# Kernel tuning notes

Hardware: AMD Instinct MI355X
Metric: run time of the kernel (lower is better)

## Reference

```python
import jax, jax.numpy as jnp
import numpy as np

B, S, D = 2, 2048, 1024
H, DH = 16, 64
EPS = 1e-5

def setup_inputs() -> dict:
    key = jax.random.key(0)
    ks = jax.random.split(key, 8)
    s = 0.02
    return {
        "x": jax.random.normal(ks[0], (B, S, D), dtype=jnp.float32),
        "ln_gamma": jnp.ones((D,), jnp.float32),
        "ln_beta": jnp.zeros((D,), jnp.float32),
        "wq": jax.random.normal(ks[1], (D, H * DH), jnp.float32) * s,
        "bq": jnp.zeros((H * DH,), jnp.float32),
        "wk": jax.random.normal(ks[2], (D, H * DH), jnp.float32) * s,
        "bk": jnp.zeros((H * DH,), jnp.float32),
        "wv": jax.random.normal(ks[3], (D, H * DH), jnp.float32) * s,
        "bv": jnp.zeros((H * DH,), jnp.float32),
        "wo": jax.random.normal(ks[4], (H * DH, D), jnp.float32) * s,
        "bo": jnp.zeros((D,), jnp.float32),
    }

def reference(x, ln_gamma, ln_beta, wq, bq, wk, bk, wv, bv, wo, bo):
    # Pre-LayerNorm over d_model
    mu = jnp.mean(x, axis=-1, keepdims=True)
    var = jnp.var(x, axis=-1, keepdims=True)
    xn = (x - mu) * jax.lax.rsqrt(var + EPS) * ln_gamma + ln_beta

    b, s, _ = xn.shape
    q = (xn @ wq + bq).reshape(b, s, H, DH)
    k = (xn @ wk + bk).reshape(b, s, H, DH)
    v = (xn @ wv + bv).reshape(b, s, H, DH)

    scale = jnp.sqrt(jnp.float32(DH))
    scores = jnp.einsum('bihd,bjhd->bhij', q, k) / scale  # [b,h,s,s]
    att = jax.nn.softmax(scores, axis=-1)
    out = jnp.einsum('bhij,bjhd->bihd', att, v).reshape(b, s, H * DH)
    return out @ wo + bo
```

## Files before the change

kernel.cpp:

```cpp
#include <hip/hip_runtime.h>
#include <math.h>

#define SEQ   2048
#define DM    1024
#define NHEAD 16
#define HD    64
#define NTOK  4096
#define EPS   1e-5f
#define SCALE_C 0.18033688f

typedef __attribute__((ext_vector_type(8))) short v8s;
typedef __attribute__((ext_vector_type(4))) short v4s;
typedef __attribute__((ext_vector_type(4))) float v4f;
typedef unsigned short ushort_t;

#define GLOAD16(g, l) __builtin_amdgcn_global_load_lds( \
    (const __attribute__((address_space(1))) unsigned int*)(g), \
    (__attribute__((address_space(3))) unsigned int*)(l), 16, 0, 0)

#if defined(__has_builtin)
#if __has_builtin(__builtin_amdgcn_mfma_f32_16x16x16_bf16)
#define MFMA16(va, vb, vc) __builtin_amdgcn_mfma_f32_16x16x16_bf16(va, vb, vc, 0, 0, 0)
#elif __has_builtin(__builtin_amdgcn_mfma_f32_16x16x16bf16_1k)
#define MFMA16(va, vb, vc) __builtin_amdgcn_mfma_f32_16x16x16bf16_1k(va, vb, vc, 0, 0, 0)
#endif
#endif
#ifndef MFMA16
__device__ __forceinline__ v4f mfma16_asm(v4s a, v4s b, v4f c) {
  asm volatile("s_nop 2\n\tv_mfma_f32_16x16x16_bf16 %0, %1, %2, %0\n\ts_nop 4"
               : "+v"(c) : "v"(a), "v"(b));
  return c;
}
#define MFMA16(va, vb, vc) mfma16_asm(va, vb, vc)
#endif

__device__ __forceinline__ unsigned short f2bf(float f) {
  union { float f; unsigned u; } v; v.f = f;
  unsigned r = v.u + 0x7FFFu + ((v.u >> 16) & 1u);
  return (unsigned short)(r >> 16);
}

__device__ __forceinline__ unsigned pack2_bf16(float a, float b) {
  union { float f; unsigned u; } ua, ub;
  ua.f = a; ub.f = b;
  return __builtin_amdgcn_perm(ub.u + 0x8000u, ua.u + 0x8000u, 0x07060302u);
}

__global__ __launch_bounds__(256) void prep_kernel(
    const float* __restrict__ x, const float* __restrict__ g,
    const float* __restrict__ be, ushort_t* __restrict__ y,
    const float* __restrict__ w0, const float* __restrict__ w1,
    const float* __restrict__ w2, const float* __restrict__ w3,
    ushort_t* __restrict__ o0, ushort_t* __restrict__ o1,
    ushort_t* __restrict__ o2, ushort_t* __restrict__ o3) {
  __shared__ float red[8];
  __shared__ float mu_s, rs_s;
  __shared__ float tile[64][65];
  const int t = threadIdx.x;
  if (blockIdx.x < NTOK) {
    const int row = blockIdx.x;
    const float4 v = ((const float4*)(x + (size_t)row * DM))[t];
    float s  = v.x + v.y + v.z + v.w;
    float ss = v.x*v.x + v.y*v.y + v.z*v.z + v.w*v.w;
    #pragma unroll
    for (int off = 32; off > 0; off >>= 1) {
      s  += __shfl_down(s,  off, 64);
      ss += __shfl_down(ss, off, 64);
    }
    const int wid = t >> 6, lane = t & 63;
    if (lane == 0) { red[wid] = s; red[4 + wid] = ss; }
    __syncthreads();
    if (t == 0) {
      const float S  = red[0] + red[1] + red[2] + red[3];
      const float SS = red[4] + red[5] + red[6] + red[7];
      const float mu  = S * (1.0f / DM);
      const float var = SS * (1.0f / DM) - mu * mu;
      mu_s = mu; rs_s = rsqrtf(var + EPS);
    }
    __syncthreads();
    const float mu = mu_s, r = rs_s;
    const float4 gv = ((const float4*)g)[t];
    const float4 bv = ((const float4*)be)[t];
    ushort4 o;
    o.x = f2bf((v.x - mu) * r * gv.x + bv.x);
    o.y = f2bf((v.y - mu) * r * gv.y + bv.y);
    o.z = f2bf((v.z - mu) * r * gv.z + bv.z);
    o.w = f2bf((v.w - mu) * r * gv.w + bv.w);
    *(ushort4*)(y + (size_t)row * DM + t * 4) = o;
  } else {
    const int i = blockIdx.x - NTOK;
    const int z = i >> 8;
    const float* w = (z==0) ? w0 : (z==1) ? w1 : (z==2) ? w2 : w3;
    ushort_t* o    = (z==0) ? o0 : (z==1) ? o1 : (z==2) ? o2 : o3;
    const int n0 = (i & 15) * 64, k0 = ((i >> 4) & 15) * 64;
    const int r = t >> 4, c4 = (t & 15) * 4;
    #pragma unroll
    for (int ii = 0; ii < 4; ++ii) {
      const float4 v = *(const float4*)(w + (size_t)(k0 + r + ii*16) * DM + n0 + c4);
      tile[r + ii*16][c4 + 0] = v.x;
      tile[r + ii*16][c4 + 1] = v.y;
      tile[r + ii*16][c4 + 2] = v.z;
      tile[r + ii*16][c4 + 3] = v.w;
    }
    __syncthreads();
    #pragma unroll
    for (int ii = 0; ii < 4; ++ii) {
      const int n = r + ii*16;
      ushort4 o4;
      o4.x = f2bf(tile[c4 + 0][n]);
      o4.y = f2bf(tile[c4 + 1][n]);
      o4.z = f2bf(tile[c4 + 2][n]);
      o4.w = f2bf(tile[c4 + 3][n]);
      *(ushort4*)(o + (size_t)(n0 + n) * DM + k0 + c4) = o4;
    }
  }
}

__device__ __forceinline__ void gemm_main(ushort_t* lsa, ushort_t* lsb,
    const ushort_t* A, const ushort_t* WT, int m0, int n0, v4f acc[4][4]) {
  const int tid = threadIdx.x;
  const int wid = tid >> 6, lane = tid & 63;
  const int mh = (wid & 1) << 6, nh = (wid >> 1) << 6;
  const int r16 = lane & 15, quad = lane >> 4;
  const int srow = lane >> 2, sch = lane & 3;
  for (int k0 = 0; k0 < DM; k0 += 64) {
    __syncthreads();
    #pragma unroll
    for (int s = 0; s < 2; ++s) {
      #pragma unroll
      for (int j = 0; j < 2; ++j) {
        const int o = wid * 2 + j;
        GLOAD16(A  + (size_t)(m0 + o*16 + srow) * DM + k0 + s*32 + sch*8, lsa + s*4096 + o*512);
        GLOAD16(WT + (size_t)(n0 + o*16 + srow) * DM + k0 + s*32 + sch*8, lsb + s*4096 + o*512);
      }
    }
    __syncthreads();
    #pragma unroll
    for (int s = 0; s < 2; ++s) {
      v8s af[4], bfr[4];
      #pragma unroll
      for (int i = 0; i < 4; ++i) {
        af[i]  = *(const v8s*)(lsa + s*4096 + (mh + i*16 + r16)*32 + quad*8);
        bfr[i] = *(const v8s*)(lsb + s*4096 + (nh + i*16 + r16)*32 + quad*8);
      }
      #pragma unroll
      for (int i = 0; i < 4; ++i)
        #pragma unroll
        for (int j = 0; j < 4; ++j)
          acc[i][j] = __builtin_amdgcn_mfma_f32_16x16x32_bf16(af[i], bfr[j], acc[i][j], 0, 0, 0);
    }
  }
}

__global__ __launch_bounds__(256, 2) void gemm_qkv(const ushort_t* __restrict__ xn,
    const ushort_t* __restrict__ wtq, const ushort_t* __restrict__ wtk, const ushort_t* __restrict__ wtv,
    const float* __restrict__ bq, const float* __restrict__ bk, const float* __restrict__ bv,
    ushort_t* __restrict__ qo, ushort_t* __restrict__ ko, ushort_t* __restrict__ vto) {
  __shared__ ushort_t lsa[128*64];
  __shared__ ushort_t lsb[128*64];
  const int flat = blockIdx.x;
  const int nf = (flat & 7) * 96 + (flat >> 3);
  const int zi = nf >> 8;
  const int yi = (nf >> 3) & 31;
  const int xi = nf & 7;
  const ushort_t* WT = (zi == 0) ? wtq : (zi == 1) ? wtk : wtv;
  const float* bias  = (zi == 0) ? bq  : (zi == 1) ? bk  : bv;
  const int m0 = yi * 128, n0 = xi * 128;
  v4f acc[4][4];
  #pragma unroll
  for (int i = 0; i < 4; ++i)
    #pragma unroll
    for (int j = 0; j < 4; ++j) acc[i][j] = (v4f){0.f, 0.f, 0.f, 0.f};
  gemm_main(lsa, lsb, xn, WT, m0, n0, acc);
  const int tid = threadIdx.x, wid = tid >> 6, lane = tid & 63;
  const int mh = (wid & 1) << 6, nh = (wid >> 1) << 6;
  const int r16 = lane & 15, quad = lane >> 4;
  if (zi < 2) {
    ushort_t* out = (zi == 0) ? qo : ko;
    const float sc = (zi == 0) ? SCALE_C : 1.0f;
    #pragma unroll
    for (int bn = 0; bn < 4; ++bn) {
      const int col = n0 + nh + bn*16 + r16;
      const float bb = bias[col];
      #pragma unroll
      for (int am = 0; am < 4; ++am) {
        const int tb = m0 + mh + am*16 + quad*4;
        #pragma unroll
        for (int r = 0; r < 4; ++r)
          out[(size_t)(tb + r) * DM + col] = f2bf((acc[am][bn][r] + bb) * sc);
      }
    }
  } else {
    #pragma unroll
    for (int bn = 0; bn < 4; ++bn) {
      const int col = n0 + nh + bn*16 + r16;
      const float bb = bias[col];
      const int h = col >> 6, d = col & 63;
      #pragma unroll
      for (int am = 0; am < 4; ++am) {
        const int tb = m0 + mh + am*16 + quad*4;
        const int b = tb >> 11, t = tb & 2047;
        const int bh = b * NHEAD + h;
        ushort4 o4;
        o4.x = f2bf(acc[am][bn][0] + bb);
        o4.y = f2bf(acc[am][bn][1] + bb);
        o4.z = f2bf(acc[am][bn][2] + bb);
        o4.w = f2bf(acc[am][bn][3] + bb);
        const size_t idx = (size_t)bh * 131072 + (size_t)(t >> 6) * 4096 +
                           (size_t)((((t >> 4) & 3) * 4) + (d >> 4)) * 256 +
                           ((t >> 2) & 3) * 64 + (d & 15) * 4;
        *(ushort4*)(vto + idx) = o4;
      }
    }
  }
}

__global__ __launch_bounds__(256, 2) void gemm_out(const ushort_t* __restrict__ A,
    const ushort_t* __restrict__ WT, const float* __restrict__ bias,
    float* __restrict__ out) {
  __shared__ ushort_t lsa[128*64];
  __shared__ ushort_t lsb[64*64];
  const int flat = blockIdx.x;
  const int nf = (flat & 7) * 64 + (flat >> 3);
  const int n0 = (nf & 15) * 64, m0 = (nf >> 4) * 128;
  const int tid = threadIdx.x;
  const int wid = tid >> 6, lane = tid & 63;
  const int mh = (wid & 1) << 6, nh = (wid >> 1) << 5;
  const int r16 = lane & 15, quad = lane >> 4;
  const int srow = lane >> 2, sch = lane & 3;
  v4f acc[4][2];
  #pragma unroll
  for (int i = 0; i < 4; ++i)
    #pragma unroll
    for (int j = 0; j < 2; ++j) acc[i][j] = (v4f){0.f, 0.f, 0.f, 0.f};
  for (int k0 = 0; k0 < DM; k0 += 64) {
    __syncthreads();
    #pragma unroll
    for (int s = 0; s < 2; ++s) {
      #pragma unroll
      for (int j = 0; j < 2; ++j) {
        const int o = wid * 2 + j;
        GLOAD16(A + (size_t)(m0 + o*16 + srow) * DM + k0 + s*32 + sch*8, lsa + s*4096 + o*512);
      }
      GLOAD16(WT + (size_t)(n0 + wid*16 + srow) * DM + k0 + s*32 + sch*8, lsb + s*2048 + wid*512);
    }
    __syncthreads();
    #pragma unroll
    for (int s = 0; s < 2; ++s) {
      v8s af[4], bfr[2];
      #pragma unroll
      for (int i = 0; i < 4; ++i)
        af[i] = *(const v8s*)(lsa + s*4096 + (mh + i*16 + r16)*32 + quad*8);
      #pragma unroll
      for (int j = 0; j < 2; ++j)
        bfr[j] = *(const v8s*)(lsb + s*2048 + (nh + j*16 + r16)*32 + quad*8);
      #pragma unroll
      for (int i = 0; i < 4; ++i)
        #pragma unroll
        for (int j = 0; j < 2; ++j)
          acc[i][j] = __builtin_amdgcn_mfma_f32_16x16x32_bf16(af[i], bfr[j], acc[i][j], 0, 0, 0);
    }
  }
  #pragma unroll
  for (int bn = 0; bn < 2; ++bn) {
    const int col = n0 + nh + bn*16 + r16;
    const float bb = bias[col];
    #pragma unroll
    for (int am = 0; am < 4; ++am) {
      const int tb = m0 + mh + am*16 + quad*4;
      #pragma unroll
      for (int r = 0; r < 4; ++r)
        out[(size_t)(tb + r) * DM + col] = acc[am][bn][r] + bb;
    }
  }
}

#define OHALF ((size_t)32 * 2048 * 64)
#define LHALF (32 * 2048)
template<int SPLIT>
__global__ __launch_bounds__(256, 8) void attn_kernel(
    const ushort_t* __restrict__ Q, const ushort_t* __restrict__ K,
    const ushort_t* __restrict__ Vt, ushort_t* __restrict__ O,
    float* __restrict__ Opart, float* __restrict__ lpart) {
  __shared__ ushort_t kbuf[8*512];
  __shared__ ushort_t vbuf[8*512];
  const int tid = threadIdx.x, wid = tid >> 6, lane = tid & 63;
  const int r16 = lane & 15, quad = lane >> 4;
  const int q0 = blockIdx.x * 64, bh = blockIdx.y;
  const int half = SPLIT ? blockIdx.z : 0;
  const int b = bh >> 4, h = bh & 15;
  const ushort_t* gQ = Q + (size_t)b * SEQ * DM + h * HD;
  const ushort_t* gK = K + (size_t)b * SEQ * DM + h * HD;
  const ushort_t* gV = Vt + (size_t)bh * 131072;

  const int qtok = q0 + wid * 16 + r16;
  const v8s qf0 = *(const v8s*)(gQ + (size_t)qtok * DM + quad * 8);
  const v8s qf1 = *(const v8s*)(gQ + (size_t)qtok * DM + 32 + quad * 8);
  v4f acco[4];
  #pragma unroll
  for (int i = 0; i < 4; ++i) acco[i] = (v4f){0.f, 0.f, 0.f, 0.f};
  float lrun = 0.f;

  const int NIT = SPLIT ? (SEQ / 128) : (SEQ / 64);
  const int kt0 = half * NIT;
  const int o0 = wid * 2, o1 = wid * 2 + 1;
  const ushort_t* srcK0 = gK + (size_t)((o0 >> 1) * 16 + r16) * DM + (o0 & 1) * 32 + quad * 8;
  const ushort_t* srcK1 = gK + (size_t)((o1 >> 1) * 16 + r16) * DM + (o1 & 1) * 32 + quad * 8;
  const ushort_t* srcV  = gV + lane * 8;

  {
    const int k0 = kt0 * 64;
    GLOAD16(srcK0 + (size_t)k0 * DM, kbuf + o0 * 512);
    GLOAD16(srcK1 + (size_t)k0 * DM, kbuf + o1 * 512);
    GLOAD16(srcV + (size_t)kt0 * 4096 + o0 * 512, vbuf + o0 * 512);
    GLOAD16(srcV + (size_t)kt0 * 4096 + o1 * 512, vbuf + o1 * 512);
  }
  __syncthreads();

  for (int it = 0; it < NIT; ++it) {
    const int kt = kt0 + it;
    uint4 rk0, rk1, rv0, rv1;
    const bool pf = (it + 1 < NIT);
    if (pf) {
      const size_t k0n = (size_t)(kt + 1) * 64;
      rk0 = *(const uint4*)(srcK0 + k0n * DM);
      rk1 = *(const uint4*)(srcK1 + k0n * DM);
      rv0 = *(const uint4*)(srcV + (size_t)(kt + 1) * 4096 + o0 * 512);
      rv1 = *(const uint4*)(srcV + (size_t)(kt + 1) * 4096 + o1 * 512);
    }

    v4f sacc[4];
    #pragma unroll
    for (int g = 0; g < 4; ++g) sacc[g] = (v4f){0.f, 0.f, 0.f, 0.f};
    #pragma unroll
    for (int g = 0; g < 4; ++g) {
      const v8s ka0 = *(const v8s*)(kbuf + (g*2 + 0) * 512 + lane * 8);
      const v8s ka1 = *(const v8s*)(kbuf + (g*2 + 1) * 512 + lane * 8);
      sacc[g] = __builtin_amdgcn_mfma_f32_16x16x32_bf16(ka0, qf0, sacc[g], 0, 0, 0);
      sacc[g] = __builtin_amdgcn_mfma_f32_16x16x32_bf16(ka1, qf1, sacc[g], 0, 0, 0);
    }

    float ls = 0.f;
    v4s pfrag[4];
    #pragma unroll
    for (int g = 0; g < 4; ++g) {
      float e0 = __builtin_amdgcn_exp2f(sacc[g][0]);
      float e1 = __builtin_amdgcn_exp2f(sacc[g][1]);
      float e2 = __builtin_amdgcn_exp2f(sacc[g][2]);
      float e3 = __builtin_amdgcn_exp2f(sacc[g][3]);
      ls += (e0 + e1) + (e2 + e3);
      union { v4s s; uint2 u; } pk;
      pk.u.x = pack2_bf16(e0, e1);
      pk.u.y = pack2_bf16(e2, e3);
      pfrag[g] = pk.s;
    }
    ls += __shfl_xor(ls, 16, 64);
    ls += __shfl_xor(ls, 32, 64);
    lrun += ls;

    #pragma unroll
    for (int dg = 0; dg < 4; ++dg) {
      #pragma unroll
      for (int g = 0; g < 4; ++g) {
        const v4s vf = *(const v4s*)(vbuf + (g*4 + dg) * 256 + quad * 64 + r16 * 4);
        acco[dg] = MFMA16(vf, pfrag[g], acco[dg]);
      }
    }

    __syncthreads();
    if (pf) {
      *(uint4*)(kbuf + o0 * 512 + lane * 8) = rk0;
      *(uint4*)(kbuf + o1 * 512 + lane * 8) = rk1;
      *(uint4*)(vbuf + o0 * 512 + lane * 8) = rv0;
      *(uint4*)(vbuf + o1 * 512 + lane * 8) = rv1;
    }
    __syncthreads();
  }

  if (SPLIT) {
    float* Op = Opart + half * OHALF + ((size_t)bh * SEQ + qtok) * 64;
    #pragma unroll
    for (int dg = 0; dg < 4; ++dg)
      *(v4f*)(Op + dg*16 + quad*4) = acco[dg];
    if (quad == 0) lpart[half * LHALF + bh * SEQ + qtok] = lrun;
  } else {
    const float inv = 1.f / lrun;
    ushort_t* gO = O + (size_t)b * SEQ * DM + h * HD;
    #pragma unroll
    for (int dg = 0; dg < 4; ++dg) {
      ushort4 o4;
      o4.x = f2bf(acco[dg][0] * inv);
      o4.y = f2bf(acco[dg][1] * inv);
      o4.z = f2bf(acco[dg][2] * inv);
      o4.w = f2bf(acco[dg][3] * inv);
      *(ushort4*)(gO + (size_t)qtok * DM + dg*16 + quad*4) = o4;
    }
  }
}

__global__ __launch_bounds__(256) void combine_kernel(
    const float* __restrict__ Opart, const float* __restrict__ lpart,
    ushort_t* __restrict__ ob) {
  const int tok = blockIdx.x;
  const int b = tok >> 11, t = tok & 2047;
  const int dm0 = threadIdx.x * 4;
  const int h = dm0 >> 6, d = dm0 & 63;
  const int bh = b * NHEAD + h;
  const size_t idx = ((size_t)bh * SEQ + t) * 64 + d;
  const float4 a = *(const float4*)(Opart + idx);
  const float4 c = *(const float4*)(Opart + OHALF + idx);
  const float l = lpart[bh * SEQ + t] + lpart[LHALF + bh * SEQ + t];
  const float inv = 1.f / l;
  ushort4 o4;
  o4.x = f2bf((a.x + c.x) * inv);
  o4.y = f2bf((a.y + c.y) * inv);
  o4.z = f2bf((a.z + c.z) * inv);
  o4.w = f2bf((a.w + c.w) * inv);
  *(ushort4*)(ob + (size_t)tok * DM + dm0) = o4;
}

extern "C" void kernel_launch(void* const* d_in, const int* in_sizes, int n_in,
                              void* d_out, int out_size, void* d_ws, size_t ws_size,
                              hipStream_t stream) {
  const float* x     = (const float*)d_in[0];
  const float* gamma = (const float*)d_in[1];
  const float* beta  = (const float*)d_in[2];
  const float* wq    = (const float*)d_in[3];
  const float* bq    = (const float*)d_in[4];
  const float* wk    = (const float*)d_in[5];
  const float* bk    = (const float*)d_in[6];
  const float* wv    = (const float*)d_in[7];
  const float* bv    = (const float*)d_in[8];
  const float* wo    = (const float*)d_in[9];
  const float* bo    = (const float*)d_in[10];
  float* out = (float*)d_out;

  unsigned char* w8 = (unsigned char*)d_ws;
  const size_t MB = 1024 * 1024;
  ushort_t* xn  = (ushort_t*)(w8 + 0 * MB);
  ushort_t* qb  = (ushort_t*)(w8 + 8 * MB);
  ushort_t* kb  = (ushort_t*)(w8 + 16 * MB);
  ushort_t* vt  = (ushort_t*)(w8 + 24 * MB);
  ushort_t* wtq = (ushort_t*)(w8 + 32 * MB);
  ushort_t* wtk = (ushort_t*)(w8 + 34 * MB);
  ushort_t* wtv = (ushort_t*)(w8 + 36 * MB);
  ushort_t* wto = (ushort_t*)(w8 + 38 * MB);
  float* Opart  = (float*)(w8 + 40 * MB);
  float* lpart  = (float*)(w8 + 72 * MB);
  ushort_t* ob  = xn;

  prep_kernel<<<dim3(NTOK + 1024), dim3(256), 0, stream>>>(
      x, gamma, beta, xn, wq, wk, wv, wo, wtq, wtk, wtv, wto);
  gemm_qkv<<<dim3(768), dim3(256), 0, stream>>>(xn, wtq, wtk, wtv, bq, bk, bv, qb, kb, vt);
  if (ws_size >= 73 * MB) {
    attn_kernel<1><<<dim3(SEQ / 64, 2 * NHEAD, 2), dim3(256), 0, stream>>>(
        qb, kb, vt, nullptr, Opart, lpart);
    combine_kernel<<<dim3(NTOK), dim3(256), 0, stream>>>(Opart, lpart, ob);
  } else {
    attn_kernel<0><<<dim3(SEQ / 64, 2 * NHEAD, 1), dim3(256), 0, stream>>>(
        qb, kb, vt, ob, nullptr, nullptr);
  }
  gemm_out<<<dim3(512), dim3(256), 0, stream>>>(ob, wto, bo, out);
}
```

Before: 207.2 us.

## Process two query tiles per wave to reuse K/V LDS loads, drop register prefetch

Each wave now handles 32 query rows (two 16-row fragments) instead of 16, so each K/V tile loaded into LDS feeds twice as many MFMAs, and the grid is halved in x. The register-staged prefetch of the next K/V tile is replaced by a direct global_load_lds at the top of each iteration, bracketed by two barriers. The occupancy hint is lowered from 8 to 4 blocks per CU to allow the larger register footprint. This halves the K/V global and LDS traffic per query, at the cost of exposing load latency each iteration, since nothing overlaps it any more, and of fewer resident waves and blocks.

```diff
diff --git a/kernel.cpp b/kernel.cpp
--- a/kernel.cpp
+++ b/kernel.cpp
@@ -278,7 +278,7 @@
 #define OHALF ((size_t)32 * 2048 * 64)
 #define LHALF (32 * 2048)
 template<int SPLIT>
-__global__ __launch_bounds__(256, 8) void attn_kernel(
+__global__ __launch_bounds__(256, 4) void attn_kernel(
     const ushort_t* __restrict__ Q, const ushort_t* __restrict__ K,
     const ushort_t* __restrict__ Vt, ushort_t* __restrict__ O,
     float* __restrict__ Opart, float* __restrict__ lpart) {
@@ -286,20 +286,26 @@
   __shared__ ushort_t vbuf[8*512];
   const int tid = threadIdx.x, wid = tid >> 6, lane = tid & 63;
   const int r16 = lane & 15, quad = lane >> 4;
-  const int q0 = blockIdx.x * 64, bh = blockIdx.y;
+  const int q0 = blockIdx.x * 128, bh = blockIdx.y;
   const int half = SPLIT ? blockIdx.z : 0;
   const int b = bh >> 4, h = bh & 15;
   const ushort_t* gQ = Q + (size_t)b * SEQ * DM + h * HD;
   const ushort_t* gK = K + (size_t)b * SEQ * DM + h * HD;
   const ushort_t* gV = Vt + (size_t)bh * 131072;
 
-  const int qtok = q0 + wid * 16 + r16;
-  const v8s qf0 = *(const v8s*)(gQ + (size_t)qtok * DM + quad * 8);
-  const v8s qf1 = *(const v8s*)(gQ + (size_t)qtok * DM + 32 + quad * 8);
-  v4f acco[4];
+  const int qt0 = q0 + wid * 32 + r16;
+  const int qt1 = qt0 + 16;
+  const v8s qf00 = *(const v8s*)(gQ + (size_t)qt0 * DM + quad * 8);
+  const v8s qf01 = *(const v8s*)(gQ + (size_t)qt0 * DM + 32 + quad * 8);
+  const v8s qf10 = *(const v8s*)(gQ + (size_t)qt1 * DM + quad * 8);
+  const v8s qf11 = *(const v8s*)(gQ + (size_t)qt1 * DM + 32 + quad * 8);
+  v4f acc0[4], acc1[4];
   #pragma unroll
-  for (int i = 0; i < 4; ++i) acco[i] = (v4f){0.f, 0.f, 0.f, 0.f};
-  float lrun = 0.f;
+  for (int i = 0; i < 4; ++i) {
+    acc0[i] = (v4f){0.f, 0.f, 0.f, 0.f};
+    acc1[i] = (v4f){0.f, 0.f, 0.f, 0.f};
+  }
+  float lrun0 = 0.f, lrun1 = 0.f;
 
   const int NIT = SPLIT ? (SEQ / 128) : (SEQ / 64);
   const int kt0 = half * NIT;
@@ -308,92 +314,102 @@
   const ushort_t* srcK1 = gK + (size_t)((o1 >> 1) * 16 + r16) * DM + (o1 & 1) * 32 + quad * 8;
   const ushort_t* srcV  = gV + lane * 8;
 
-  {
-    const int k0 = kt0 * 64;
+  for (int it = 0; it < NIT; ++it) {
+    const int kt = kt0 + it;
+    const int k0 = kt * 64;
+    __syncthreads();
     GLOAD16(srcK0 + (size_t)k0 * DM, kbuf + o0 * 512);
     GLOAD16(srcK1 + (size_t)k0 * DM, kbuf + o1 * 512);
-    GLOAD16(srcV + (size_t)kt0 * 4096 + o0 * 512, vbuf + o0 * 512);
-    GLOAD16(srcV + (size_t)kt0 * 4096 + o1 * 512, vbuf + o1 * 512);
-  }
-  __syncthreads();
-
-  for (int it = 0; it < NIT; ++it) {
-    const int kt = kt0 + it;
-    uint4 rk0, rk1, rv0, rv1;
-    const bool pf = (it + 1 < NIT);
-    if (pf) {
-      const size_t k0n = (size_t)(kt + 1) * 64;
-      rk0 = *(const uint4*)(srcK0 + k0n * DM);
-      rk1 = *(const uint4*)(srcK1 + k0n * DM);
-      rv0 = *(const uint4*)(srcV + (size_t)(kt + 1) * 4096 + o0 * 512);
-      rv1 = *(const uint4*)(srcV + (size_t)(kt + 1) * 4096 + o1 * 512);
-    }
-
-    v4f sacc[4];
-    #pragma unroll
-    for (int g = 0; g < 4; ++g) sacc[g] = (v4f){0.f, 0.f, 0.f, 0.f};
+    GLOAD16(srcV + (size_t)kt * 4096 + o0 * 512, vbuf + o0 * 512);
+    GLOAD16(srcV + (size_t)kt * 4096 + o1 * 512, vbuf + o1 * 512);
+    __syncthreads();
+
+    v4f s0[4], s1[4];
+    #pragma unroll
+    for (int g = 0; g < 4; ++g) {
+      s0[g] = (v4f){0.f, 0.f, 0.f, 0.f};
+      s1[g] = (v4f){0.f, 0.f, 0.f, 0.f};
+    }
     #pragma unroll
     for (int g = 0; g < 4; ++g) {
       const v8s ka0 = *(const v8s*)(kbuf + (g*2 + 0) * 512 + lane * 8);
       const v8s ka1 = *(const v8s*)(kbuf + (g*2 + 1) * 512 + lane * 8);
-      sacc[g] = __builtin_amdgcn_mfma_f32_16x16x32_bf16(ka0, qf0, sacc[g], 0, 0, 0);
-      sacc[g] = __builtin_amdgcn_mfma_f32_16x16x32_bf16(ka1, qf1, sacc[g], 0, 0, 0);
-    }
-
-    float ls = 0.f;
-    v4s pfrag[4];
+      s0[g] = __builtin_amdgcn_mfma_f32_16x16x32_bf16(ka0, qf00, s0[g], 0, 0, 0);
+      s0[g] = __builtin_amdgcn_mfma_f32_16x16x32_bf16(ka1, qf01, s0[g], 0, 0, 0);
+      s1[g] = __builtin_amdgcn_mfma_f32_16x16x32_bf16(ka0, qf10, s1[g], 0, 0, 0);
+      s1[g] = __builtin_amdgcn_mfma_f32_16x16x32_bf16(ka1, qf11, s1[g], 0, 0, 0);
+    }
+
+    v4s pf0[4], pf1[4];
+    float ls0 = 0.f, ls1 = 0.f;
     #pragma unroll
     for (int g = 0; g < 4; ++g) {
-      float e0 = __builtin_amdgcn_exp2f(sacc[g][0]);
-      float e1 = __builtin_amdgcn_exp2f(sacc[g][1]);
-      float e2 = __builtin_amdgcn_exp2f(sacc[g][2]);
-      float e3 = __builtin_amdgcn_exp2f(sacc[g][3]);
-      ls += (e0 + e1) + (e2 + e3);
+      float e0 = __builtin_amdgcn_exp2f(s0[g][0]);
+      float e1 = __builtin_amdgcn_exp2f(s0[g][1]);
+      float e2 = __builtin_amdgcn_exp2f(s0[g][2]);
+      float e3 = __builtin_amdgcn_exp2f(s0[g][3]);
+      ls0 += (e0 + e1) + (e2 + e3);
       union { v4s s; uint2 u; } pk;
       pk.u.x = pack2_bf16(e0, e1);
       pk.u.y = pack2_bf16(e2, e3);
-      pfrag[g] = pk.s;
-    }
-    ls += __shfl_xor(ls, 16, 64);
-    ls += __shfl_xor(ls, 32, 64);
-    lrun += ls;
+      pf0[g] = pk.s;
+      float f0 = __builtin_amdgcn_exp2f(s1[g][0]);
+      float f1 = __builtin_amdgcn_exp2f(s1[g][1]);
+      float f2 = __builtin_amdgcn_exp2f(s1[g][2]);
+      float f3 = __builtin_amdgcn_exp2f(s1[g][3]);
+      ls1 += (f0 + f1) + (f2 + f3);
+      union { v4s s; uint2 u; } pk2;
+      pk2.u.x = pack2_bf16(f0, f1);
+      pk2.u.y = pack2_bf16(f2, f3);
+      pf1[g] = pk2.s;
+    }
+    ls0 += __shfl_xor(ls0, 16, 64);
+    ls0 += __shfl_xor(ls0, 32, 64);
+    lrun0 += ls0;
+    ls1 += __shfl_xor(ls1, 16, 64);
+    ls1 += __shfl_xor(ls1, 32, 64);
+    lrun1 += ls1;
 
     #pragma unroll
     for (int dg = 0; dg < 4; ++dg) {
       #pragma unroll
       for (int g = 0; g < 4; ++g) {
         const v4s vf = *(const v4s*)(vbuf + (g*4 + dg) * 256 + quad * 64 + r16 * 4);
-        acco[dg] = MFMA16(vf, pfrag[g], acco[dg]);
-      }
-    }
-
-    __syncthreads();
-    if (pf) {
-      *(uint4*)(kbuf + o0 * 512 + lane * 8) = rk0;
-      *(uint4*)(kbuf + o1 * 512 + lane * 8) = rk1;
-      *(uint4*)(vbuf + o0 * 512 + lane * 8) = rv0;
-      *(uint4*)(vbuf + o1 * 512 + lane * 8) = rv1;
-    }
-    __syncthreads();
+        acc0[dg] = MFMA16(vf, pf0[g], acc0[dg]);
+        acc1[dg] = MFMA16(vf, pf1[g], acc1[dg]);
+      }
+    }
   }
 
   if (SPLIT) {
-    float* Op = Opart + half * OHALF + ((size_t)bh * SEQ + qtok) * 64;
-    #pragma unroll
-    for (int dg = 0; dg < 4; ++dg)
-      *(v4f*)(Op + dg*16 + quad*4) = acco[dg];
-    if (quad == 0) lpart[half * LHALF + bh * SEQ + qtok] = lrun;
+    float* Op0 = Opart + half * OHALF + ((size_t)bh * SEQ + qt0) * 64;
+    float* Op1 = Opart + half * OHALF + ((size_t)bh * SEQ + qt1) * 64;
+    #pragma unroll
+    for (int dg = 0; dg < 4; ++dg) {
+      *(v4f*)(Op0 + dg*16 + quad*4) = acc0[dg];
+      *(v4f*)(Op1 + dg*16 + quad*4) = acc1[dg];
+    }
+    if (quad == 0) {
+      lpart[half * LHALF + bh * SEQ + qt0] = lrun0;
+      lpart[half * LHALF + bh * SEQ + qt1] = lrun1;
+    }
   } else {
-    const float inv = 1.f / lrun;
+    const float inv0 = 1.f / lrun0, inv1 = 1.f / lrun1;
     ushort_t* gO = O + (size_t)b * SEQ * DM + h * HD;
     #pragma unroll
     for (int dg = 0; dg < 4; ++dg) {
       ushort4 o4;
-      o4.x = f2bf(acco[dg][0] * inv);
-      o4.y = f2bf(acco[dg][1] * inv);
-      o4.z = f2bf(acco[dg][2] * inv);
-      o4.w = f2bf(acco[dg][3] * inv);
-      *(ushort4*)(gO + (size_t)qtok * DM + dg*16 + quad*4) = o4;
+      o4.x = f2bf(acc0[dg][0] * inv0);
+      o4.y = f2bf(acc0[dg][1] * inv0);
+      o4.z = f2bf(acc0[dg][2] * inv0);
+      o4.w = f2bf(acc0[dg][3] * inv0);
+      *(ushort4*)(gO + (size_t)qt0 * DM + dg*16 + quad*4) = o4;
+      ushort4 o5;
+      o5.x = f2bf(acc1[dg][0] * inv1);
+      o5.y = f2bf(acc1[dg][1] * inv1);
+      o5.z = f2bf(acc1[dg][2] * inv1);
+      o5.w = f2bf(acc1[dg][3] * inv1);
+      *(ushort4*)(gO + (size_t)qt1 * DM + dg*16 + quad*4) = o5;
     }
   }
 }
@@ -453,11 +469,11 @@
       x, gamma, beta, xn, wq, wk, wv, wo, wtq, wtk, wtv, wto);
   gemm_qkv<<<dim3(768), dim3(256), 0, stream>>>(xn, wtq, wtk, wtv, bq, bk, bv, qb, kb, vt);
   if (ws_size >= 73 * MB) {
-    attn_kernel<1><<<dim3(SEQ / 64, 2 * NHEAD, 2), dim3(256), 0, stream>>>(
+    attn_kernel<1><<<dim3(SEQ / 128, 2 * NHEAD, 2), dim3(256), 0, stream>>>(
         qb, kb, vt, nullptr, Opart, lpart);
     combine_kernel<<<dim3(NTOK), dim3(256), 0, stream>>>(Opart, lpart, ob);
   } else {
-    attn_kernel<0><<<dim3(SEQ / 64, 2 * NHEAD, 1), dim3(256), 0, stream>>>(
+    attn_kernel<0><<<dim3(SEQ / 128, 2 * NHEAD, 1), dim3(256), 0, stream>>>(
         qb, kb, vt, ob, nullptr, nullptr);
   }
   gemm_out<<<dim3(512), dim3(256), 0, stream>>>(ob, wto, bo, out);
```

Result: faster. 199.1 us (-3.9%).
